# Performance work log

Hardware: AMD Instinct MI355X
Metric: run time of the kernel (lower is better)

The kernel has to match this reference:

```python
import jax, jax.numpy as jnp
import numpy as np

N = 100000
E = 1600000
C = 192      # in_channels
GH = 256     # grapher hidden
FH = 512     # ffn hidden
EPS = 1e-5


def _bn(x, gamma, beta):
    # BatchNorm1d, training-mode batch statistics over the node axis
    mean = jnp.mean(x, axis=0)
    var = jnp.var(x, axis=0)
    return (x - mean) * jax.lax.rsqrt(var + EPS) * gamma + beta


def setup_inputs() -> dict:
    key = jax.random.key(0)
    ks = jax.random.split(key, 12)
    s = 0.02
    inp = {
        "x": jax.random.normal(ks[0], (N, C), dtype=jnp.float32),
        "edge_index": jax.random.randint(ks[1], (2, E), 0, N, dtype=jnp.int64),
        # Grapher fc1
        "Wg1": jax.random.normal(ks[2], (C, GH), jnp.float32) * s,
        "bg1": jnp.zeros((GH,), jnp.float32),
        "gg1": jnp.ones((GH,), jnp.float32),
        "beg1": jnp.zeros((GH,), jnp.float32),
        # GraphConv (lin_rel has bias, lin_root no bias, per PyG)
        "Wrel": jax.random.normal(ks[3], (GH, GH), jnp.float32) * s,
        "brel": jnp.zeros((GH,), jnp.float32),
        "Wroot": jax.random.normal(ks[4], (GH, GH), jnp.float32) * s,
        # Grapher fc2
        "Wg2": jax.random.normal(ks[5], (GH, C), jnp.float32) * s,
        "bg2": jnp.zeros((C,), jnp.float32),
        "gg2": jnp.ones((C,), jnp.float32),
        "beg2": jnp.zeros((C,), jnp.float32),
        # FFN fc1
        "Wf1": jax.random.normal(ks[6], (C, FH), jnp.float32) * s,
        "bf1": jnp.zeros((FH,), jnp.float32),
        "gf1": jnp.ones((FH,), jnp.float32),
        "bef1": jnp.zeros((FH,), jnp.float32),
        # FFN fc2
        "Wf2": jax.random.normal(ks[7], (FH, C), jnp.float32) * s,
        "bf2": jnp.zeros((C,), jnp.float32),
        "gf2": jnp.ones((C,), jnp.float32),
        "bef2": jnp.zeros((C,), jnp.float32),
    }
    return inp


def reference(x, edge_index, Wg1, bg1, gg1, beg1, Wrel, brel, Wroot,
              Wg2, bg2, gg2, beg2, Wf1, bf1, gf1, bef1, Wf2, bf2, gf2, bef2):
    n = x.shape[0]
    src, dst = edge_index[0], edge_index[1]

    # ---- Grapher ----
    shortcut = x
    h = _bn(x @ Wg1 + bg1, gg1, beg1)                       # [N, GH]
    # GraphConv: sum-aggregate neighbor messages at target nodes
    agg = jax.ops.segment_sum(h[src], dst, num_segments=n)  # [N, GH]
    gc = agg @ Wrel + brel + h @ Wroot
    h = jax.nn.gelu(gc, approximate=False)
    h = _bn(h @ Wg2 + bg2, gg2, beg2)                       # [N, C]
    x = h + shortcut

    # ---- FFN ----
    shortcut = x
    h = jax.nn.gelu(_bn(x @ Wf1 + bf1, gf1, bef1), approximate=False)
    h = _bn(h @ Wf2 + bf2, gf2, bef2)
    return h + shortcut
```

## Files before the change

kernel.cpp:

```cpp
#include <hip/hip_runtime.h>
#include <math.h>

typedef __bf16 bf16x8 __attribute__((ext_vector_type(8)));
typedef float  floatx4 __attribute__((ext_vector_type(4)));

__device__ inline float bf_lo(unsigned u){ return __uint_as_float(u << 16); }
__device__ inline float bf_hi(unsigned u){ return __uint_as_float(u & 0xffff0000u); }
__device__ inline unsigned short f2bf_u(float f){
    unsigned u = __float_as_uint(f);
    return (unsigned short)((u + 0x7fffu + ((u >> 16) & 1u)) >> 16);
}
__device__ inline unsigned pack2(float a, float b){
    return (unsigned)f2bf_u(a) | ((unsigned)f2bf_u(b) << 16);
}
__device__ inline float gelu_f(float v){
    return 0.5f * v * (1.f + erff(v * 0.70710678118654752f));
}
__device__ inline void gload_lds16(const void* g, void* l){
    __builtin_amdgcn_global_load_lds(
        (const __attribute__((address_space(1))) unsigned int*)g,
        (__attribute__((address_space(3))) unsigned int*)l, 16, 0, 0);
}

__global__ void zero_k(int* __restrict__ p, int n){
    int i = blockIdx.x * 256 + threadIdx.x;
    if (i < n) p[i] = 0;
}

__global__ void xcast_k(const float* __restrict__ x, unsigned short* __restrict__ xb, long n8){
    long i = (long)blockIdx.x * 256 + threadIdx.x;
    if (i < n8){
        const float4* p = (const float4*)(x + i * 8);
        float4 a = p[0], b = p[1];
        uint4 o;
        o.x = pack2(a.x, a.y); o.y = pack2(a.z, a.w);
        o.z = pack2(b.x, b.y); o.w = pack2(b.z, b.w);
        *(uint4*)(xb + i * 8) = o;
    }
}

__global__ void wprep_k(const float* __restrict__ W, unsigned short* __restrict__ Wt,
                        int K, int Ncols, int ostride, int ooffs){
    int idx = blockIdx.x * 256 + threadIdx.x;
    if (idx < K * Ncols){
        int k = idx / Ncols, n = idx - k * Ncols;
        Wt[(size_t)n * ostride + ooffs + k] = f2bf_u(W[idx]);
    }
}

__global__ void mkbn_k(const float* __restrict__ gsum, const float* __restrict__ gsq,
                       const float* __restrict__ gamma, const float* __restrict__ beta,
                       float* __restrict__ scv, float* __restrict__ shv, int C_, float invN){
    int c = blockIdx.x * 256 + threadIdx.x;
    if (c < C_){
        float mean = gsum[c] * invN;
        float var  = gsq[c] * invN - mean * mean;
        float sc   = gamma[c] * rsqrtf(var + 1e-5f);
        scv[c] = sc;
        shv[c] = beta[c] - mean * sc;
    }
}

__global__ void wscale_k(unsigned short* __restrict__ wt, const float* __restrict__ scv, int total){
    int i = blockIdx.x * 256 + threadIdx.x;
    if (i < total){
        float v = __uint_as_float(((unsigned)wt[i]) << 16);
        wt[i] = f2bf_u(v * scv[i & 255]);
    }
}

__global__ void biasrr_k(const float* __restrict__ Wrel, const float* __restrict__ Wroot,
                         const float* __restrict__ brel, const float* __restrict__ shv,
                         float* __restrict__ bias2, float* __restrict__ rvec){
    int m = threadIdx.x;
    float b2 = 0.f, rv = 0.f;
    for (int k = 0; k < 256; ++k){
        float s = shv[k];
        rv = fmaf(s, Wrel[k * 256 + m], rv);
        b2 = fmaf(s, Wroot[k * 256 + m], b2);
    }
    bias2[m] = brel[m] + b2;
    rvec[m]  = rv;
}

#define RBSH 9
#define RB   512
#define PCH  8192

__global__ __launch_bounds__(256)
void bhist_k(const int* __restrict__ dst, int* __restrict__ bcnt, int E){
    __shared__ int h[256];
    for (int i = threadIdx.x; i < 256; i += 256) h[i] = 0;
    __syncthreads();
    for (long i = (long)blockIdx.x * 256 + threadIdx.x; i < E; i += (long)gridDim.x * 256)
        atomicAdd(&h[dst[i] >> RBSH], 1);
    __syncthreads();
    int v = h[threadIdx.x];
    if (v) atomicAdd(&bcnt[threadIdx.x * 16], v);
}

__global__ void bscan_k(const int* __restrict__ bcnt, int* __restrict__ bbase,
                        int* __restrict__ bcur, int nbuk, int E){
    __shared__ int s[256];
    const int t = threadIdx.x;
    int v = (t < nbuk) ? bcnt[t * 16] : 0;
    s[t] = v; __syncthreads();
    for (int d = 1; d < 256; d <<= 1){
        int tt = (t >= d) ? s[t - d] : 0;
        __syncthreads();
        s[t] += tt;
        __syncthreads();
    }
    int excl = s[t] - v;
    if (t < nbuk){ bbase[t] = excl; bcur[t * 16] = excl; }
    if (t == 0) bbase[nbuk] = E;
}

__global__ __launch_bounds__(512)
void bpart_k(const int* __restrict__ src, const int* __restrict__ dst,
             int* __restrict__ bcur, int2* __restrict__ pairs, int E){
    __shared__ int h[256];
    __shared__ int s[256];
    __shared__ int cur[256];
    const int t = threadIdx.x;
    const int base = blockIdx.x * PCH;
    const int cnt = min(PCH, E - base);
    if (t < 256) h[t] = 0;
    __syncthreads();
    for (int i = t; i < cnt; i += 512)
        atomicAdd(&h[dst[base + i] >> RBSH], 1);
    __syncthreads();
    if (t < 256) s[t] = h[t];
    __syncthreads();
    for (int d = 1; d < 256; d <<= 1){
        int tt = 0;
        if (t < 256 && t >= d) tt = s[t - d];
        __syncthreads();
        if (t < 256) s[t] += tt;
        __syncthreads();
    }
    if (t < 256){
        int myc = h[t];
        int g = 0;
        if (myc) g = atomicAdd(&bcur[t * 16], myc);
        cur[t] = g;
    }
    __syncthreads();
    for (int i = t; i < cnt; i += 512){
        int d = dst[base + i];
        int b = d >> RBSH;
        int r = atomicAdd(&cur[b], 1);
        pairs[r] = make_int2(src[base + i], d);
    }
}

__global__ __launch_bounds__(1024)
void bbuild_k(const int2* __restrict__ pairs, const int* __restrict__ bbase,
              int* __restrict__ offsets, int* __restrict__ esrc, int N, int E){
    __shared__ int h[RB];
    __shared__ int s[RB];
    const int b = blockIdx.x;
    const int t = threadIdx.x;
    const int p0 = bbase[b], p1 = bbase[b + 1];
    if (t < RB) h[t] = 0;
    __syncthreads();
    for (int i = p0 + t; i < p1; i += 1024)
        atomicAdd(&h[pairs[i].y & (RB - 1)], 1);
    __syncthreads();
    int v = 0;
    if (t < RB){ v = h[t]; s[t] = v; }
    __syncthreads();
    for (int d = 1; d < RB; d <<= 1){
        int tt = 0;
        if (t < RB && t >= d) tt = s[t - d];
        __syncthreads();
        if (t < RB) s[t] += tt;
        __syncthreads();
    }
    if (t < RB){
        int node = (b << RBSH) + t;
        int excl = p0 + s[t] - v;
        if (node < N) offsets[node] = excl;
        h[t] = excl;
    }
    __syncthreads();
    for (int i = p0 + t; i < p1; i += 1024){
        int2 pr = pairs[i];
        int r = atomicAdd(&h[pr.y & (RB - 1)], 1);
        esrc[r] = pr.x;
    }
    if (b == 0 && t == 0) offsets[N] = E;
}

__global__ __launch_bounds__(256)
void agg_k(const unsigned short* __restrict__ hbn, const int* __restrict__ offsets,
           const int* __restrict__ esrc, unsigned short* __restrict__ aggout, int N){
    const int lane = threadIdx.x & 63;
    const int node = blockIdx.x * 4 + (threadIdx.x >> 6);
    if (node >= N) return;
    const int off  = offsets[node];
    const int end  = offsets[node + 1];
    const int half = lane >> 5;
    const int l32  = lane & 31;
    float a[8];
#pragma unroll
    for (int j = 0; j < 8; ++j) a[j] = 0.f;
    const unsigned short* hb = hbn + l32 * 8;
    for (int c = off; c < end; c += 64){
        const int e = c + lane;
        int sl = (e < end) ? esrc[e] : 0;
        const int cnt = min(64, end - c);
        for (int j = 0; j < cnt; j += 16){
            int   s[8];
            float m[8];
            uint4 u[8];
#pragma unroll
            for (int k = 0; k < 8; ++k){
                const int idx = j + 2 * k + half;
                s[k] = __shfl(sl, idx);
                m[k] = (idx < cnt) ? 1.f : 0.f;
            }
#pragma unroll
            for (int k = 0; k < 8; ++k)
                u[k] = *(const uint4*)(hb + (size_t)s[k] * 512);
#pragma unroll
            for (int k = 0; k < 8; ++k){
                a[0] = fmaf(m[k], bf_lo(u[k].x), a[0]);
                a[1] = fmaf(m[k], bf_hi(u[k].x), a[1]);
                a[2] = fmaf(m[k], bf_lo(u[k].y), a[2]);
                a[3] = fmaf(m[k], bf_hi(u[k].y), a[3]);
                a[4] = fmaf(m[k], bf_lo(u[k].z), a[4]);
                a[5] = fmaf(m[k], bf_hi(u[k].z), a[5]);
                a[6] = fmaf(m[k], bf_lo(u[k].w), a[6]);
                a[7] = fmaf(m[k], bf_hi(u[k].w), a[7]);
            }
        }
    }
#pragma unroll
    for (int j = 0; j < 8; ++j)
        a[j] += __shfl_xor(a[j], 32);
    if (half == 0){
        uint4 o;
        o.x = pack2(a[0], a[1]); o.y = pack2(a[2], a[3]);
        o.z = pack2(a[4], a[5]); o.w = pack2(a[6], a[7]);
        *(uint4*)(aggout + (size_t)node * 512 + l32 * 8) = o;
    }
}

template<int K, bool GELU_OUT, bool STATS, bool DEGBIAS>
__global__ __launch_bounds__(256)
void gemm3_k(const unsigned short* __restrict__ A, const unsigned short* __restrict__ Bt,
             const float* __restrict__ bias, unsigned short* __restrict__ Cp,
             long M, int ostride, int ooffs,
             float* __restrict__ gsum, float* __restrict__ gsq,
             const int* __restrict__ offs, const float* __restrict__ rvec){
    __shared__ unsigned short Xs[128 * 64];
    __shared__ unsigned short Ws[64 * 64];
    const int t    = threadIdx.x;
    const int lane = t & 63;
    const int w    = t >> 6;
    const int r16  = lane & 15;
    const int q4   = lane >> 4;
    const long mbase = (long)blockIdx.x * 128;
    const int  cb    = blockIdx.y * 64;

    floatx4 acc[4][2];
#pragma unroll
    for (int ai = 0; ai < 4; ++ai)
#pragma unroll
        for (int bi = 0; bi < 2; ++bi) acc[ai][bi] = (floatx4)0.f;

    const int lrow = w * 8 + (lane >> 3);
    const int lk   = (lane & 7) * 8;
    const unsigned short* ga = A  + (size_t)(mbase + lrow) * K + lk;
    const unsigned short* gb = Bt + (size_t)(cb + lrow) * K + lk;
    unsigned short* lx = Xs + w * 512 + lane * 8;
    unsigned short* lw = Ws + w * 512 + lane * 8;

    for (int kt = 0; kt < K; kt += 64){
#pragma unroll
        for (int i = 0; i < 4; ++i)
            gload_lds16(ga + (size_t)i * 32 * K + kt, lx + i * 2048);
#pragma unroll
        for (int j = 0; j < 2; ++j)
            gload_lds16(gb + (size_t)j * 32 * K + kt, lw + j * 2048);
        asm volatile("s_waitcnt vmcnt(0)" ::: "memory");
        __syncthreads();
#pragma unroll
        for (int kc = 0; kc < 64; kc += 32){
            bf16x8 wf[4], xf[2];
#pragma unroll
            for (int ai = 0; ai < 4; ++ai)
                wf[ai] = *(const bf16x8*)(Ws + (ai * 16 + r16) * 64 + kc + q4 * 8);
#pragma unroll
            for (int bi = 0; bi < 2; ++bi)
                xf[bi] = *(const bf16x8*)(Xs + (w * 32 + bi * 16 + r16) * 64 + kc + q4 * 8);
#pragma unroll
            for (int ai = 0; ai < 4; ++ai)
#pragma unroll
                for (int bi = 0; bi < 2; ++bi)
                    acc[ai][bi] = __builtin_amdgcn_mfma_f32_16x16x32_bf16(
                        wf[ai], xf[bi], acc[ai][bi], 0, 0, 0);
        }
        __syncthreads();
    }

    float4 bv[4];
#pragma unroll
    for (int ai = 0; ai < 4; ++ai)
        bv[ai] = *(const float4*)(bias + cb + ai * 16 + q4 * 4);
    float4 rv[4];
    if constexpr (DEGBIAS){
#pragma unroll
        for (int ai = 0; ai < 4; ++ai)
            rv[ai] = *(const float4*)(rvec + cb + ai * 16 + q4 * 4);
    }
    float cs[4][4], cq[4][4];
    if constexpr (STATS){
#pragma unroll
        for (int ai = 0; ai < 4; ++ai)
#pragma unroll
            for (int j = 0; j < 4; ++j){ cs[ai][j] = 0.f; cq[ai][j] = 0.f; }
    }
#pragma unroll
    for (int bi = 0; bi < 2; ++bi){
        long node = mbase + w * 32 + bi * 16 + r16;
        const bool valid = node < M;
        float degf = 0.f;
        if constexpr (DEGBIAS){
            if (valid) degf = (float)(offs[node + 1] - offs[node]);
        }
        unsigned short* cp = Cp + (size_t)node * ostride + ooffs + cb;
#pragma unroll
        for (int ai = 0; ai < 4; ++ai){
            float v[4];
            v[0] = acc[ai][bi][0] + bv[ai].x;
            v[1] = acc[ai][bi][1] + bv[ai].y;
            v[2] = acc[ai][bi][2] + bv[ai].z;
            v[3] = acc[ai][bi][3] + bv[ai].w;
            if constexpr (DEGBIAS){
                v[0] = fmaf(degf, rv[ai].x, v[0]);
                v[1] = fmaf(degf, rv[ai].y, v[1]);
                v[2] = fmaf(degf, rv[ai].z, v[2]);
                v[3] = fmaf(degf, rv[ai].w, v[3]);
            }
            if constexpr (STATS){
#pragma unroll
                for (int j = 0; j < 4; ++j){
                    float vv = valid ? v[j] : 0.f;
                    cs[ai][j] += vv;
                    cq[ai][j] = fmaf(vv, vv, cq[ai][j]);
                }
            }
            if constexpr (GELU_OUT){
                v[0] = gelu_f(v[0]); v[1] = gelu_f(v[1]);
                v[2] = gelu_f(v[2]); v[3] = gelu_f(v[3]);
            }
            if (valid){
                uint2 o; o.x = pack2(v[0], v[1]); o.y = pack2(v[2], v[3]);
                *(uint2*)(cp + ai * 16 + q4 * 4) = o;
            }
        }
    }

    if constexpr (STATS){
#pragma unroll
        for (int ai = 0; ai < 4; ++ai)
#pragma unroll
            for (int j = 0; j < 4; ++j){
#pragma unroll
                for (int m = 1; m < 16; m <<= 1){
                    cs[ai][j] += __shfl_xor(cs[ai][j], m);
                    cq[ai][j] += __shfl_xor(cq[ai][j], m);
                }
            }
        float* ssum = (float*)Xs;
        float* ssq  = ssum + 256;
        if (r16 == 0){
#pragma unroll
            for (int ai = 0; ai < 4; ++ai)
#pragma unroll
                for (int j = 0; j < 4; ++j){
                    ssum[w * 64 + ai * 16 + q4 * 4 + j] = cs[ai][j];
                    ssq [w * 64 + ai * 16 + q4 * 4 + j] = cq[ai][j];
                }
        }
        __syncthreads();
        if (t < 64){
            float s = 0.f, q = 0.f;
#pragma unroll
            for (int ww = 0; ww < 4; ++ww){ s += ssum[ww * 64 + t]; q += ssq[ww * 64 + t]; }
            atomicAdd(&gsum[cb + t], s);
            atomicAdd(&gsq [cb + t], q);
        }
    }
}

template<int NCOLS, bool GELU_OUT, bool RES, bool RES_F32, bool OUT_F32>
__global__ __launch_bounds__(256)
void bn_apply_k(const unsigned short* __restrict__ in, void* __restrict__ outv,
                const void* __restrict__ resv,
                const float* __restrict__ gsum, const float* __restrict__ gsq,
                const float* __restrict__ gamma, const float* __restrict__ beta,
                long nrows, int ostride, int ooffs, float invN){
    __shared__ float s_scale[NCOLS], s_shift[NCOLS];
    for (int c = threadIdx.x; c < NCOLS; c += 256){
        float mean = gsum[c] * invN;
        float var  = gsq[c] * invN - mean * mean;
        float sc   = gamma[c] * rsqrtf(var + 1e-5f);
        s_scale[c] = sc;
        s_shift[c] = beta[c] - mean * sc;
    }
    __syncthreads();
    long i8 = ((long)blockIdx.x * 256 + threadIdx.x) * 8;
    if (i8 >= nrows * (long)NCOLS) return;
    long row  = i8 / NCOLS;
    int  col0 = (int)(i8 - row * NCOLS);
    uint4 u = *(const uint4*)(in + i8);
    float v[8];
    v[0] = bf_lo(u.x); v[1] = bf_hi(u.x); v[2] = bf_lo(u.y); v[3] = bf_hi(u.y);
    v[4] = bf_lo(u.z); v[5] = bf_hi(u.z); v[6] = bf_lo(u.w); v[7] = bf_hi(u.w);
#pragma unroll
    for (int j = 0; j < 8; ++j){
        v[j] = v[j] * s_scale[col0 + j] + s_shift[col0 + j];
        if constexpr (GELU_OUT) v[j] = gelu_f(v[j]);
    }
    if constexpr (RES){
        if constexpr (RES_F32){
            const float4* rp = (const float4*)((const float*)resv + i8);
            float4 r0 = rp[0], r1 = rp[1];
            v[0] += r0.x; v[1] += r0.y; v[2] += r0.z; v[3] += r0.w;
            v[4] += r1.x; v[5] += r1.y; v[6] += r1.z; v[7] += r1.w;
        } else {
            uint4 r = *(const uint4*)((const unsigned short*)resv + i8);
            v[0] += bf_lo(r.x); v[1] += bf_hi(r.x); v[2] += bf_lo(r.y); v[3] += bf_hi(r.y);
            v[4] += bf_lo(r.z); v[5] += bf_hi(r.z); v[6] += bf_lo(r.w); v[7] += bf_hi(r.w);
        }
    }
    long opos = row * ostride + ooffs + col0;
    if constexpr (OUT_F32){
        float4* op = (float4*)((float*)outv + opos);
        op[0] = make_float4(v[0], v[1], v[2], v[3]);
        op[1] = make_float4(v[4], v[5], v[6], v[7]);
    } else {
        uint4 o;
        o.x = pack2(v[0], v[1]); o.y = pack2(v[2], v[3]);
        o.z = pack2(v[4], v[5]); o.w = pack2(v[6], v[7]);
        *(uint4*)((unsigned short*)outv + opos) = o;
    }
}

extern "C" void kernel_launch(void* const* d_in, const int* in_sizes, int n_in,
                              void* d_out, int out_size, void* d_ws, size_t ws_size,
                              hipStream_t stream){
    const int C = 192, GH = 256, FH = 512;
    const float* x    = (const float*)d_in[0];
    const int*   ei   = (const int*)d_in[1];
    const float* Wg1  = (const float*)d_in[2];
    const float* bg1  = (const float*)d_in[3];
    const float* gg1  = (const float*)d_in[4];
    const float* beg1 = (const float*)d_in[5];
    const float* Wrel = (const float*)d_in[6];
    const float* brel = (const float*)d_in[7];
    const float* Wroot= (const float*)d_in[8];
    const float* Wg2  = (const float*)d_in[9];
    const float* bg2  = (const float*)d_in[10];
    const float* gg2  = (const float*)d_in[11];
    const float* beg2 = (const float*)d_in[12];
    const float* Wf1  = (const float*)d_in[13];
    const float* bf1  = (const float*)d_in[14];
    const float* gf1  = (const float*)d_in[15];
    const float* bef1 = (const float*)d_in[16];
    const float* Wf2  = (const float*)d_in[17];
    const float* bf2  = (const float*)d_in[18];
    const float* gf2  = (const float*)d_in[19];
    const float* bef2 = (const float*)d_in[20];

    const int N = in_sizes[0] / C;
    const int E = in_sizes[1] / 2;
    const int* e_src = ei;
    const int* e_dst = ei + E;

    char* wp = (char*)d_ws;
    auto carve = [&](size_t bytes) -> void* {
        void* p = (void*)wp; wp += (bytes + 255) & ~(size_t)255; return p;
    };
    unsigned short* wt_g1 = (unsigned short*)carve((size_t)GH * C * 2);
    unsigned short* wt_rr = (unsigned short*)carve((size_t)GH * 512 * 2);
    unsigned short* wt_g2 = (unsigned short*)carve((size_t)C * GH * 2);
    unsigned short* wt_f1 = (unsigned short*)carve((size_t)FH * C * 2);
    unsigned short* wt_f2 = (unsigned short*)carve((size_t)C * FH * 2);
    float* stats = (float*)carve(2 * (size_t)(GH + C + FH + C) * 4);
    float* sum1 = stats;        float* sq1 = sum1 + GH;
    float* sum2 = sq1 + GH;     float* sq2 = sum2 + C;
    float* sum3 = sq2 + C;      float* sq3 = sum3 + FH;
    float* sum4 = sq3 + FH;     float* sq4 = sum4 + C;
    float* scv   = (float*)carve(256 * 4);
    float* shv   = (float*)carve(256 * 4);
    float* bias2 = (float*)carve(256 * 4);
    float* rvec  = (float*)carve(256 * 4);
    unsigned short* buf0  = (unsigned short*)carve((size_t)N * 512 * 2);
    unsigned short* bufAG = (unsigned short*)carve((size_t)N * 512 * 2);
    int* offsets = (int*)carve((size_t)(N + 1) * 4);
    int* esrc    = (int*)carve((size_t)E * 4);
    int* bcnt    = (int*)carve((size_t)256 * 16 * 4);
    int* bbase   = (int*)carve((size_t)257 * 4);
    int* bcur    = (int*)carve((size_t)256 * 16 * 4);
    int2* pairs = (int2*)buf0;
    unsigned short* x_bf = buf0;
    unsigned short* g    = buf0;
    unsigned short* f1   = buf0;
    unsigned short* AG   = bufAG;
    unsigned short* h2   = bufAG;
    unsigned short* h4   = bufAG + (size_t)N * C;
    (void)ws_size; (void)n_in; (void)out_size;

    const float invN = 1.0f / (float)N;
    const int GB = (N + 127) / 128;
    const int nbuk = (N + RB - 1) >> RBSH;

    wprep_k<<<(C * GH + 255) / 256, 256, 0, stream>>>(Wg1, wt_g1, C, GH, C, 0);
    wprep_k<<<(GH * GH + 255) / 256, 256, 0, stream>>>(Wrel, wt_rr, GH, GH, 512, 0);
    wprep_k<<<(GH * GH + 255) / 256, 256, 0, stream>>>(Wroot, wt_rr, GH, GH, 512, GH);
    wprep_k<<<(GH * C + 255) / 256, 256, 0, stream>>>(Wg2, wt_g2, GH, C, GH, 0);
    wprep_k<<<(C * FH + 255) / 256, 256, 0, stream>>>(Wf1, wt_f1, C, FH, C, 0);
    wprep_k<<<(FH * C + 255) / 256, 256, 0, stream>>>(Wf2, wt_f2, FH, C, FH, 0);

    const int nstats = 2 * (GH + C + FH + C);
    zero_k<<<(nstats + 255) / 256, 256, 0, stream>>>((int*)stats, nstats);
    zero_k<<<(256 * 16 + 255) / 256, 256, 0, stream>>>(bcnt, 256 * 16);

    bhist_k<<<1024, 256, 0, stream>>>(e_dst, bcnt, E);
    bscan_k<<<1, 256, 0, stream>>>(bcnt, bbase, bcur, nbuk, E);
    bpart_k<<<(E + PCH - 1) / PCH, 512, 0, stream>>>(e_src, e_dst, bcur, pairs, E);
    bbuild_k<<<nbuk, 1024, 0, stream>>>(pairs, bbase, offsets, esrc, N, E);

    xcast_k<<<(int)(((size_t)N * C / 8 + 255) / 256), 256, 0, stream>>>(x, x_bf, (long)N * C / 8);

    gemm3_k<192, false, true, false><<<dim3(GB, GH / 64), 256, 0, stream>>>(
        x_bf, wt_g1, bg1, AG, N, 512, 256, sum1, sq1, nullptr, nullptr);
    mkbn_k<<<1, 256, 0, stream>>>(sum1, sq1, gg1, beg1, scv, shv, GH, invN);
    wscale_k<<<(GH * 512 + 255) / 256, 256, 0, stream>>>(wt_rr, scv, GH * 512);
    biasrr_k<<<1, 256, 0, stream>>>(Wrel, Wroot, brel, shv, bias2, rvec);
    agg_k<<<(N + 3) / 4, 256, 0, stream>>>(AG + 256, offsets, esrc, AG, N);
    gemm3_k<512, true, false, true><<<dim3(GB, GH / 64), 256, 0, stream>>>(
        AG, wt_rr, bias2, g, N, GH, 0, nullptr, nullptr, offsets, rvec);
    gemm3_k<256, false, true, false><<<dim3(GB, C / 64), 256, 0, stream>>>(
        g, wt_g2, bg2, h2, N, C, 0, sum2, sq2, nullptr, nullptr);
    bn_apply_k<192, false, true, true, false><<<(int)(((size_t)N * C / 8 + 255) / 256), 256, 0, stream>>>(
        h2, h2, x, sum2, sq2, gg2, beg2, N, 192, 0, invN);

    gemm3_k<192, false, true, false><<<dim3(GB, FH / 64), 256, 0, stream>>>(
        h2, wt_f1, bf1, f1, N, FH, 0, sum3, sq3, nullptr, nullptr);
    bn_apply_k<512, true, false, false, false><<<(int)(((size_t)N * FH / 8 + 255) / 256), 256, 0, stream>>>(
        f1, f1, nullptr, sum3, sq3, gf1, bef1, N, 512, 0, invN);
    gemm3_k<512, false, true, false><<<dim3(GB, C / 64), 256, 0, stream>>>(
        f1, wt_f2, bf2, h4, N, C, 0, sum4, sq4, nullptr, nullptr);
    bn_apply_k<192, false, true, false, true><<<(int)(((size_t)N * C / 8 + 255) / 256), 256, 0, stream>>>(
        h4, d_out, h2, sum4, sq4, gf2, bef2, N, 192, 0, invN);
}
```

Baseline: 903.1 us.

## Remap GEMM workgroups per XCD and replace stat atomics with partial-sum reduction

The GEMM grid becomes 1D, and block IDs are remapped so consecutive tiles land on the same XCD, improving L2 locality on the multi-die GPU. Column statistics are now written as per-row-block partial sums and reduced by a new colreduce kernel, replacing global float atomics and the stats zeroing launch. The serial 256-iteration biasrr loop is split across 8 blocks with atomics, with mkbn initialising the outputs. This adds extra launches and partial-sum buffer traffic in exchange for less atomic contention and better cache reuse.

```diff
diff --git a/kernel.cpp b/kernel.cpp
--- a/kernel.cpp
+++ b/kernel.cpp
@@ -50,7 +50,10 @@
 
 __global__ void mkbn_k(const float* __restrict__ gsum, const float* __restrict__ gsq,
                        const float* __restrict__ gamma, const float* __restrict__ beta,
-                       float* __restrict__ scv, float* __restrict__ shv, int C_, float invN){
+                       const float* __restrict__ brel,
+                       float* __restrict__ scv, float* __restrict__ shv,
+                       float* __restrict__ bias2, float* __restrict__ rvec,
+                       int C_, float invN){
     int c = blockIdx.x * 256 + threadIdx.x;
     if (c < C_){
         float mean = gsum[c] * invN;
@@ -58,6 +61,8 @@
         float sc   = gamma[c] * rsqrtf(var + 1e-5f);
         scv[c] = sc;
         shv[c] = beta[c] - mean * sc;
+        bias2[c] = brel[c];
+        rvec[c]  = 0.f;
     }
 }
 
@@ -70,17 +75,18 @@
 }
 
 __global__ void biasrr_k(const float* __restrict__ Wrel, const float* __restrict__ Wroot,
-                         const float* __restrict__ brel, const float* __restrict__ shv,
+                         const float* __restrict__ shv,
                          float* __restrict__ bias2, float* __restrict__ rvec){
     int m = threadIdx.x;
+    int k0 = blockIdx.x * 32;
     float b2 = 0.f, rv = 0.f;
-    for (int k = 0; k < 256; ++k){
+    for (int k = k0; k < k0 + 32; ++k){
         float s = shv[k];
         rv = fmaf(s, Wrel[k * 256 + m], rv);
         b2 = fmaf(s, Wroot[k * 256 + m], b2);
     }
-    bias2[m] = brel[m] + b2;
-    rvec[m]  = rv;
+    atomicAdd(&bias2[m], b2);
+    atomicAdd(&rvec[m],  rv);
 }
 
 #define RBSH 9
@@ -247,13 +253,13 @@
     }
 }
 
-template<int K, bool GELU_OUT, bool STATS, bool DEGBIAS>
+template<int K, bool GELU_OUT, bool DEGBIAS, bool STATS>
 __global__ __launch_bounds__(256)
 void gemm3_k(const unsigned short* __restrict__ A, const unsigned short* __restrict__ Bt,
              const float* __restrict__ bias, unsigned short* __restrict__ Cp,
-             long M, int ostride, int ooffs,
-             float* __restrict__ gsum, float* __restrict__ gsq,
-             const int* __restrict__ offs, const float* __restrict__ rvec){
+             long M, int NY, int ostride, int ooffs,
+             const int* __restrict__ offs, const float* __restrict__ rvec,
+             float* __restrict__ psum, float* __restrict__ psq){
     __shared__ unsigned short Xs[128 * 64];
     __shared__ unsigned short Ws[64 * 64];
     const int t    = threadIdx.x;
@@ -261,8 +267,16 @@
     const int w    = t >> 6;
     const int r16  = lane & 15;
     const int q4   = lane >> 4;
-    const long mbase = (long)blockIdx.x * 128;
-    const int  cb    = blockIdx.y * 64;
+
+    const int nwg  = gridDim.x;
+    const int orig = blockIdx.x;
+    const int qq   = nwg >> 3, rr = nwg & 7;
+    const int xcd  = orig & 7, kk = orig >> 3;
+    const int wgid = (xcd < rr ? xcd * (qq + 1) : rr * (qq + 1) + (xcd - rr) * qq) + kk;
+    const int xb   = wgid / NY;
+    const int yb   = wgid - xb * NY;
+    const long mbase = (long)xb * 128;
+    const int  cb    = yb * 64;
 
     floatx4 acc[4][2];
 #pragma unroll
@@ -333,31 +347,28 @@
         unsigned short* cp = Cp + (size_t)node * ostride + ooffs + cb;
 #pragma unroll
         for (int ai = 0; ai < 4; ++ai){
-            float v[4];
-            v[0] = acc[ai][bi][0] + bv[ai].x;
-            v[1] = acc[ai][bi][1] + bv[ai].y;
-            v[2] = acc[ai][bi][2] + bv[ai].z;
-            v[3] = acc[ai][bi][3] + bv[ai].w;
+            float v0 = acc[ai][bi][0] + bv[ai].x;
+            float v1 = acc[ai][bi][1] + bv[ai].y;
+            float v2 = acc[ai][bi][2] + bv[ai].z;
+            float v3 = acc[ai][bi][3] + bv[ai].w;
             if constexpr (DEGBIAS){
-                v[0] = fmaf(degf, rv[ai].x, v[0]);
-                v[1] = fmaf(degf, rv[ai].y, v[1]);
-                v[2] = fmaf(degf, rv[ai].z, v[2]);
-                v[3] = fmaf(degf, rv[ai].w, v[3]);
+                v0 = fmaf(degf, rv[ai].x, v0);
+                v1 = fmaf(degf, rv[ai].y, v1);
+                v2 = fmaf(degf, rv[ai].z, v2);
+                v3 = fmaf(degf, rv[ai].w, v3);
             }
             if constexpr (STATS){
-#pragma unroll
-                for (int j = 0; j < 4; ++j){
-                    float vv = valid ? v[j] : 0.f;
-                    cs[ai][j] += vv;
-                    cq[ai][j] = fmaf(vv, vv, cq[ai][j]);
-                }
+                float mm = valid ? 1.f : 0.f;
+                cs[ai][0] += mm * v0; cq[ai][0] = fmaf(mm * v0, v0, cq[ai][0]);
+                cs[ai][1] += mm * v1; cq[ai][1] = fmaf(mm * v1, v1, cq[ai][1]);
+                cs[ai][2] += mm * v2; cq[ai][2] = fmaf(mm * v2, v2, cq[ai][2]);
+                cs[ai][3] += mm * v3; cq[ai][3] = fmaf(mm * v3, v3, cq[ai][3]);
             }
             if constexpr (GELU_OUT){
-                v[0] = gelu_f(v[0]); v[1] = gelu_f(v[1]);
-                v[2] = gelu_f(v[2]); v[3] = gelu_f(v[3]);
+                v0 = gelu_f(v0); v1 = gelu_f(v1); v2 = gelu_f(v2); v3 = gelu_f(v3);
             }
             if (valid){
-                uint2 o; o.x = pack2(v[0], v[1]); o.y = pack2(v[2], v[3]);
+                uint2 o; o.x = pack2(v0, v1); o.y = pack2(v2, v3);
                 *(uint2*)(cp + ai * 16 + q4 * 4) = o;
             }
         }
@@ -390,10 +401,33 @@
             float s = 0.f, q = 0.f;
 #pragma unroll
             for (int ww = 0; ww < 4; ++ww){ s += ssum[ww * 64 + t]; q += ssq[ww * 64 + t]; }
-            atomicAdd(&gsum[cb + t], s);
-            atomicAdd(&gsq [cb + t], q);
-        }
-    }
+            const int nc = NY * 64;
+            psum[(size_t)xb * nc + cb + t] = s;
+            psq [(size_t)xb * nc + cb + t] = q;
+        }
+    }
+}
+
+__global__ void colreduce_k(const float* __restrict__ ps, const float* __restrict__ pq,
+                            float* __restrict__ gsum, float* __restrict__ gsq,
+                            int ncols, int nxb){
+    __shared__ float ss[256], sq_[256];
+    const int c = blockIdx.x;
+    float s = 0.f, q = 0.f;
+    for (int i = threadIdx.x; i < nxb; i += 256){
+        s += ps[(size_t)i * ncols + c];
+        q += pq[(size_t)i * ncols + c];
+    }
+    ss[threadIdx.x] = s; sq_[threadIdx.x] = q;
+    __syncthreads();
+    for (int d = 128; d > 0; d >>= 1){
+        if (threadIdx.x < d){
+            ss[threadIdx.x]  += ss[threadIdx.x + d];
+            sq_[threadIdx.x] += sq_[threadIdx.x + d];
+        }
+        __syncthreads();
+    }
+    if (threadIdx.x == 0){ gsum[c] = ss[0]; gsq[c] = sq_[0]; }
 }
 
 template<int NCOLS, bool GELU_OUT, bool RES, bool RES_F32, bool OUT_F32>
@@ -499,6 +533,9 @@
     float* shv   = (float*)carve(256 * 4);
     float* bias2 = (float*)carve(256 * 4);
     float* rvec  = (float*)carve(256 * 4);
+    const int GB = (N + 127) / 128;
+    float* psum = (float*)carve((size_t)GB * 512 * 4);
+    float* psq  = (float*)carve((size_t)GB * 512 * 4);
     unsigned short* buf0  = (unsigned short*)carve((size_t)N * 512 * 2);
     unsigned short* bufAG = (unsigned short*)carve((size_t)N * 512 * 2);
     int* offsets = (int*)carve((size_t)(N + 1) * 4);
@@ -516,7 +553,6 @@
     (void)ws_size; (void)n_in; (void)out_size;
 
     const float invN = 1.0f / (float)N;
-    const int GB = (N + 127) / 128;
     const int nbuk = (N + RB - 1) >> RBSH;
 
     wprep_k<<<(C * GH + 255) / 256, 256, 0, stream>>>(Wg1, wt_g1, C, GH, C, 0);
@@ -526,8 +562,6 @@
     wprep_k<<<(C * FH + 255) / 256, 256, 0, stream>>>(Wf1, wt_f1, C, FH, C, 0);
     wprep_k<<<(FH * C + 255) / 256, 256, 0, stream>>>(Wf2, wt_f2, FH, C, FH, 0);
 
-    const int nstats = 2 * (GH + C + FH + C);
-    zero_k<<<(nstats + 255) / 256, 256, 0, stream>>>((int*)stats, nstats);
     zero_k<<<(256 * 16 + 255) / 256, 256, 0, stream>>>(bcnt, 256 * 16);
 
     bhist_k<<<1024, 256, 0, stream>>>(e_dst, bcnt, E);
@@ -537,25 +571,29 @@
 
     xcast_k<<<(int)(((size_t)N * C / 8 + 255) / 256), 256, 0, stream>>>(x, x_bf, (long)N * C / 8);
 
-    gemm3_k<192, false, true, false><<<dim3(GB, GH / 64), 256, 0, stream>>>(
-        x_bf, wt_g1, bg1, AG, N, 512, 256, sum1, sq1, nullptr, nullptr);
-    mkbn_k<<<1, 256, 0, stream>>>(sum1, sq1, gg1, beg1, scv, shv, GH, invN);
+    gemm3_k<192, false, false, true><<<GB * (GH / 64), 256, 0, stream>>>(
+        x_bf, wt_g1, bg1, AG, N, GH / 64, 512, 256, nullptr, nullptr, psum, psq);
+    colreduce_k<<<GH, 256, 0, stream>>>(psum, psq, sum1, sq1, GH, GB);
+    mkbn_k<<<1, 256, 0, stream>>>(sum1, sq1, gg1, beg1, brel, scv, shv, bias2, rvec, GH, invN);
     wscale_k<<<(GH * 512 + 255) / 256, 256, 0, stream>>>(wt_rr, scv, GH * 512);
-    biasrr_k<<<1, 256, 0, stream>>>(Wrel, Wroot, brel, shv, bias2, rvec);
+    biasrr_k<<<8, 256, 0, stream>>>(Wrel, Wroot, shv, bias2, rvec);
     agg_k<<<(N + 3) / 4, 256, 0, stream>>>(AG + 256, offsets, esrc, AG, N);
-    gemm3_k<512, true, false, true><<<dim3(GB, GH / 64), 256, 0, stream>>>(
-        AG, wt_rr, bias2, g, N, GH, 0, nullptr, nullptr, offsets, rvec);
-    gemm3_k<256, false, true, false><<<dim3(GB, C / 64), 256, 0, stream>>>(
-        g, wt_g2, bg2, h2, N, C, 0, sum2, sq2, nullptr, nullptr);
+    gemm3_k<512, true, true, false><<<GB * (GH / 64), 256, 0, stream>>>(
+        AG, wt_rr, bias2, g, N, GH / 64, GH, 0, offsets, rvec, nullptr, nullptr);
+    gemm3_k<256, false, false, true><<<GB * (C / 64), 256, 0, stream>>>(
+        g, wt_g2, bg2, h2, N, C / 64, C, 0, nullptr, nullptr, psum, psq);
+    colreduce_k<<<C, 256, 0, stream>>>(psum, psq, sum2, sq2, C, GB);
     bn_apply_k<192, false, true, true, false><<<(int)(((size_t)N * C / 8 + 255) / 256), 256, 0, stream>>>(
         h2, h2, x, sum2, sq2, gg2, beg2, N, 192, 0, invN);
 
-    gemm3_k<192, false, true, false><<<dim3(GB, FH / 64), 256, 0, stream>>>(
-        h2, wt_f1, bf1, f1, N, FH, 0, sum3, sq3, nullptr, nullptr);
+    gemm3_k<192, false, false, true><<<GB * (FH / 64), 256, 0, stream>>>(
+        h2, wt_f1, bf1, f1, N, FH / 64, FH, 0, nullptr, nullptr, psum, psq);
+    colreduce_k<<<FH, 256, 0, stream>>>(psum, psq, sum3, sq3, FH, GB);
     bn_apply_k<512, true, false, false, false><<<(int)(((size_t)N * FH / 8 + 255) / 256), 256, 0, stream>>>(
         f1, f1, nullptr, sum3, sq3, gf1, bef1, N, 512, 0, invN);
-    gemm3_k<512, false, true, false><<<dim3(GB, C / 64), 256, 0, stream>>>(
-        f1, wt_f2, bf2, h4, N, C, 0, sum4, sq4, nullptr, nullptr);
+    gemm3_k<512, false, false, true><<<GB * (C / 64), 256, 0, stream>>>(
+        f1, wt_f2, bf2, h4, N, C / 64, C, 0, nullptr, nullptr, psum, psq);
+    colreduce_k<<<C, 256, 0, stream>>>(psum, psq, sum4, sq4, C, GB);
     bn_apply_k<192, false, true, false, true><<<(int)(((size_t)N * C / 8 + 255) / 256), 256, 0, stream>>>(
         h4, d_out, h2, sum4, sq4, gf2, bef2, N, 192, 0, invN);
 }
```

Result: faster. 768.8 us (-14.9%).
